# Kernel optimization log

Measured on AMD Instinct MI355X. Metric: run time of the kernel, lower is better.

## Reference

```python
import jax, jax.numpy as jnp
import numpy as np

EMB = 512
HEADS = 8
HEAD_DIM = EMB // HEADS


def setup_inputs() -> dict:
    key = jax.random.key(0)
    ks = jax.random.split(key, 8)
    S, B = 2048, 2
    q = jax.random.normal(ks[0], (S, B, EMB), dtype=jnp.float32)
    k = jax.random.normal(ks[1], (S, B, EMB), dtype=jnp.float32)
    v = jax.random.normal(ks[2], (S, B, EMB), dtype=jnp.float32)
    sc = 1.0 / np.sqrt(HEAD_DIM)
    Wq = jax.random.normal(ks[3], (HEAD_DIM, HEAD_DIM), dtype=jnp.float32) * sc
    Wk = jax.random.normal(ks[4], (HEAD_DIM, HEAD_DIM), dtype=jnp.float32) * sc
    Wv = jax.random.normal(ks[5], (HEAD_DIM, HEAD_DIM), dtype=jnp.float32) * sc
    Wfc = jax.random.normal(ks[6], (EMB, EMB), dtype=jnp.float32) * (1.0 / np.sqrt(EMB))
    bfc = jax.random.normal(ks[7], (EMB,), dtype=jnp.float32) * 0.01
    return {"q": q, "k": k, "v": v, "Wq": Wq, "Wk": Wk, "Wv": Wv, "Wfc": Wfc, "bfc": bfc}


def reference(q, k, v, Wq, Wk, Wv, Wfc, bfc):
    query_len, batch, emb = q.shape
    key_len = k.shape[0]
    value_len = v.shape[0]
    # Faithful to the original: plain reshape (NOT transpose) from [S,B,E] -> [B,H,S,D]
    qh = q.reshape(batch, HEADS, query_len, HEAD_DIM)
    kh = k.reshape(batch, HEADS, key_len, HEAD_DIM)
    vh = v.reshape(batch, HEADS, value_len, HEAD_DIM)
    # torch Linear(head_dim, head_dim, bias=False): y = x @ W.T
    Q = qh @ Wq.T
    K = kh @ Wk.T
    V = vh @ Wv.T
    QK = jnp.einsum('bhqd,bhkd->bhqk', Q, K)  # [B,H,S,S] score matrix (memory-bound)
    filt = jax.nn.softmax(QK / np.sqrt(HEAD_DIM).astype(np.float32), axis=3)
    att = jnp.einsum('bhqk,bhkd->bhqd', filt, V)
    att = att.reshape(query_len, batch, emb)
    return att @ Wfc.T + bfc
```

## Files before the change

### kernel.cpp

```cpp
#include <hip/hip_runtime.h>


typedef __attribute__((ext_vector_type(8))) __bf16 bf16x8;
typedef __attribute__((ext_vector_type(4))) float f32x4;
typedef __attribute__((ext_vector_type(4))) unsigned short u16x4;
typedef __attribute__((ext_vector_type(4))) unsigned int u32x4;
typedef unsigned short u16;
typedef unsigned int u32;

static __device__ __forceinline__ u16 f2bf(float x) {
    u32 u = __float_as_uint(x);
    u += 0x7fff + ((u >> 16) & 1);
    return (u16)(u >> 16);
}
static __device__ __forceinline__ float bf2f(u16 h) {
    return __uint_as_float(((u32)h) << 16);
}
static __device__ __forceinline__ u32 pack2bf(float lo, float hi) {
    u32 a = __float_as_uint(lo), b = __float_as_uint(hi);
    a += 0x7fff + ((a >> 16) & 1);
    b += 0x7fff + ((b >> 16) & 1);
    return (a >> 16) | (b & 0xffff0000u);
}

__global__ __launch_bounds__(256) void proj_kernel(
    const float* __restrict__ q, const float* __restrict__ k, const float* __restrict__ v,
    const float* __restrict__ Wq, const float* __restrict__ Wk, const float* __restrict__ Wv,
    const float* __restrict__ Wfc,
    u16* __restrict__ Qb, u16* __restrict__ Kb, u16* __restrict__ Vt,
    u16* __restrict__ Wb, float* __restrict__ KnSq)
{
    const int mode = blockIdx.z;
    const int t = threadIdx.x;

    if (mode == 3) {
        int i = (blockIdx.x * 256 + t) * 4;
        float4 val = *(const float4*)(Wfc + i);
        u16x4 b = { f2bf(val.x), f2bf(val.y), f2bf(val.z), f2bf(val.w) };
        *(u16x4*)(Wb + i) = b;
        return;
    }

    const float* A = (mode == 0) ? q : (mode == 1) ? k : v;
    const float* W = (mode == 0) ? Wq : (mode == 1) ? Wk : Wv;
    const float osc = (mode == 0) ? 0.18033688011112042f : 1.0f;

    __shared__ alignas(16) u16 Ash[128 * 88];
    __shared__ alignas(16) u16 Wsh[64 * 88];
    __shared__ float red[128];

    const int m0 = blockIdx.x * 128;
    const int w = t >> 6, l = t & 63;
    const int r16 = l & 15, q4 = l >> 4;

    {
        const float4* A4 = (const float4*)(A + (size_t)m0 * 64);
        const int c4 = t & 15;
        #pragma unroll
        for (int i = 0; i < 8; ++i) {
            int row = (t >> 4) + i * 16;
            float4 val = A4[row * 16 + c4];
            u16x4 bb = { f2bf(val.x), f2bf(val.y), f2bf(val.z), f2bf(val.w) };
            *(u16x4*)(Ash + row * 88 + c4 * 4) = bb;
        }
        const float4* W4 = (const float4*)W;
        #pragma unroll
        for (int i = 0; i < 4; ++i) {
            int row = (t >> 4) + i * 16;
            float4 val = W4[row * 16 + c4];
            u16x4 bb = { f2bf(val.x), f2bf(val.y), f2bf(val.z), f2bf(val.w) };
            *(u16x4*)(Wsh + row * 88 + c4 * 4) = bb;
        }
    }
    __syncthreads();

    bf16x8 af[2][2], wf[4][2];
    #pragma unroll
    for (int mc = 0; mc < 2; ++mc)
        #pragma unroll
        for (int kk = 0; kk < 2; ++kk)
            af[mc][kk] = *(const bf16x8*)(Ash + (w * 32 + mc * 16 + r16) * 88 + kk * 32 + q4 * 8);
    #pragma unroll
    for (int nc = 0; nc < 4; ++nc)
        #pragma unroll
        for (int kk = 0; kk < 2; ++kk)
            wf[nc][kk] = *(const bf16x8*)(Wsh + (nc * 16 + r16) * 88 + kk * 32 + q4 * 8);

    f32x4 acc[2][4];
    const f32x4 zero = {0.f, 0.f, 0.f, 0.f};
    #pragma unroll
    for (int mc = 0; mc < 2; ++mc)
        #pragma unroll
        for (int nc = 0; nc < 4; ++nc) {
            acc[mc][nc] = zero;
            acc[mc][nc] = __builtin_amdgcn_mfma_f32_16x16x32_bf16(af[mc][0], wf[nc][0], acc[mc][nc], 0, 0, 0);
            acc[mc][nc] = __builtin_amdgcn_mfma_f32_16x16x32_bf16(af[mc][1], wf[nc][1], acc[mc][nc], 0, 0, 0);
        }

    __syncthreads();

    if (mode < 2) {
        #pragma unroll
        for (int mc = 0; mc < 2; ++mc)
            #pragma unroll
            for (int nc = 0; nc < 4; ++nc)
                #pragma unroll
                for (int r = 0; r < 4; ++r)
                    Ash[(w * 32 + mc * 16 + q4 * 4 + r) * 72 + nc * 16 + r16] = f2bf(acc[mc][nc][r] * osc);
        __syncthreads();
        u16* Out = ((mode == 0) ? Qb : Kb) + (size_t)m0 * 64;
        {
            int row = t >> 1, cbase = (t & 1) * 32;
            #pragma unroll
            for (int i = 0; i < 4; ++i)
                *(u32x4*)(Out + row * 64 + cbase + i * 8) = *(const u32x4*)(Ash + row * 72 + cbase + i * 8);
        }
        if (mode == 1) {
            if (t < 128) {
                float ss = 0.f;
                #pragma unroll
                for (int c = 0; c < 8; ++c) {
                    u32x4 d = *(const u32x4*)(Ash + t * 72 + c * 8);
                    #pragma unroll
                    for (int j = 0; j < 4; ++j) {
                        float lo = bf2f((u16)(d[j] & 0xffff));
                        float hi = bf2f((u16)(d[j] >> 16));
                        ss += lo * lo + hi * hi;
                    }
                }
                red[t] = ss;
            }
            __syncthreads();
            if (t < 64) red[t] = fmaxf(red[t], red[t + 64]);
            __syncthreads();
            if (t < 32) red[t] = fmaxf(red[t], red[t + 32]);
            __syncthreads();
            if (t == 0) {
                float mx = red[0];
                for (int i = 1; i < 32; ++i) mx = fmaxf(mx, red[i]);
                KnSq[blockIdx.x] = mx;
            }
        }
    } else {
        #pragma unroll
        for (int mc = 0; mc < 2; ++mc)
            #pragma unroll
            for (int nc = 0; nc < 4; ++nc)
                #pragma unroll
                for (int r = 0; r < 4; ++r)
                    Ash[(nc * 16 + r16) * 136 + w * 32 + mc * 16 + q4 * 4 + r] = f2bf(acc[mc][nc][r]);
        __syncthreads();
        const int g = m0 >> 11, s0 = m0 & 2047;
        int d = t >> 2, sb = (t & 3) * 32;
        u16* Out = Vt + ((size_t)(g * 64 + d)) * 2048 + s0;
        #pragma unroll
        for (int i = 0; i < 4; ++i)
            *(u32x4*)(Out + sb + i * 8) = *(const u32x4*)(Ash + d * 136 + sb + i * 8);
    }
}

__global__ __launch_bounds__(256) void flash_kernel(
    const u16* __restrict__ Qb, const u16* __restrict__ Kb,
    const u16* __restrict__ Vt, const float* __restrict__ KnSq,
    u16* __restrict__ Att)
{
    const int g = blockIdx.y;
    const int qt = blockIdx.x;
    const int t = threadIdx.x, w = t >> 6, l = t & 63;
    const int r16 = l & 15, q4 = l >> 4;
    const int r7 = r16 & 7;

    __shared__ alignas(16) u16 Kt[2][64 * 64];
    __shared__ alignas(16) u16 Vs[2][64 * 64];
    __shared__ alignas(16) u16 Psh[4][16 * 64];

    const u16* Kg = Kb + ((size_t)g) * 2048 * 64;
    const u16* Vg = Vt + ((size_t)g) * 64 * 2048;

    bf16x8 qb[2];
    {
        const u16* qp = Qb + ((size_t)(g * 2048 + qt * 64 + w * 16 + r16)) * 64 + q4 * 8;
        qb[0] = *(const bf16x8*)qp;
        qb[1] = *(const bf16x8*)(qp + 32);
    }

    float m;
    {
        float kss = KnSq[g * 16 + r16];
        kss = fmaxf(kss, __shfl_xor(kss, 1));
        kss = fmaxf(kss, __shfl_xor(kss, 2));
        kss = fmaxf(kss, __shfl_xor(kss, 4));
        kss = fmaxf(kss, __shfl_xor(kss, 8));
        float ss = 0.f;
        #pragma unroll
        for (int kk = 0; kk < 2; ++kk)
            #pragma unroll
            for (int j = 0; j < 8; ++j) {
                float x = (float)qb[kk][j];
                ss += x * x;
            }
        ss += __shfl_xor(ss, 16);
        ss += __shfl_xor(ss, 32);
        m = sqrtf(ss) * sqrtf(kss) * 1.0002f;
    }

    const int rr = t >> 3, ck = t & 7;
    const int sw0 = (ck ^ (rr & 7)) * 8;

    {
        #pragma unroll
        for (int h = 0; h < 2; ++h) {
            int row = h * 32 + rr;
            *(u32x4*)(&Kt[0][row * 64 + sw0]) = *(const u32x4*)(Kg + (size_t)row * 64 + ck * 8);
            *(u32x4*)(&Vs[0][row * 64 + sw0]) = *(const u32x4*)(Vg + (size_t)row * 2048 + ck * 8);
        }
    }
    __syncthreads();

    f32x4 o[4];
    const f32x4 zero = {0.f, 0.f, 0.f, 0.f};
    #pragma unroll
    for (int dc = 0; dc < 4; ++dc) o[dc] = zero;
    float lsum = 0.f;

    u16* pw = &Psh[w][r16 * 64];
    const int pq_off = (q4 & 1) * 4;
    const int fr0 = ((q4 ^ r7)) * 8;
    const int fr1 = (((q4 + 4) & 7) ^ r7) * 8;

    for (int it = 0; it < 32; ++it) {
        const int cur = it & 1;
        const bool hasn = (it < 31);

        u32x4 knx[2], vnx[2];
        if (hasn) {
            #pragma unroll
            for (int h = 0; h < 2; ++h) {
                int row = h * 32 + rr;
                knx[h] = *(const u32x4*)(Kg + (size_t)((it + 1) * 64 + row) * 64 + ck * 8);
                vnx[h] = *(const u32x4*)(Vg + (size_t)row * 2048 + (it + 1) * 64 + ck * 8);
            }
        }

        const u16* Kc = Kt[cur];
        const u16* Vc = Vs[cur];
        bf16x8 ka[4][2], va[4][2];
        #pragma unroll
        for (int kc = 0; kc < 4; ++kc) {
            ka[kc][0] = *(const bf16x8*)(Kc + (kc * 16 + r16) * 64 + fr0);
            ka[kc][1] = *(const bf16x8*)(Kc + (kc * 16 + r16) * 64 + fr1);
        }
        #pragma unroll
        for (int dc = 0; dc < 4; ++dc) {
            va[dc][0] = *(const bf16x8*)(Vc + (dc * 16 + r16) * 64 + fr0);
            va[dc][1] = *(const bf16x8*)(Vc + (dc * 16 + r16) * 64 + fr1);
        }

        f32x4 s[4];
        #pragma unroll
        for (int kc = 0; kc < 4; ++kc) {
            s[kc] = zero;
            s[kc] = __builtin_amdgcn_mfma_f32_16x16x32_bf16(ka[kc][0], qb[0], s[kc], 0, 0, 0);
            s[kc] = __builtin_amdgcn_mfma_f32_16x16x32_bf16(ka[kc][1], qb[1], s[kc], 0, 0, 0);
        }

        float p[4][4];
        float psum = 0.f;
        #pragma unroll
        for (int kc = 0; kc < 4; ++kc)
            #pragma unroll
            for (int r = 0; r < 4; ++r) {
                p[kc][r] = exp2f(s[kc][r] - m);
                psum += p[kc][r];
            }
        lsum += psum;

        #pragma unroll
        for (int kc = 0; kc < 4; ++kc) {
            uint2 dd = { pack2bf(p[kc][0], p[kc][1]), pack2bf(p[kc][2], p[kc][3]) };
            int sc = ((2 * kc + (q4 >> 1)) ^ r7) * 8 + pq_off;
            *(uint2*)(pw + sc) = dd;
        }
        bf16x8 pb0 = *(const bf16x8*)(pw + fr0);
        bf16x8 pb1 = *(const bf16x8*)(pw + fr1);

        #pragma unroll
        for (int dc = 0; dc < 4; ++dc) {
            o[dc] = __builtin_amdgcn_mfma_f32_16x16x32_bf16(va[dc][0], pb0, o[dc], 0, 0, 0);
            o[dc] = __builtin_amdgcn_mfma_f32_16x16x32_bf16(va[dc][1], pb1, o[dc], 0, 0, 0);
        }

        if (hasn) {
            const int nxt = cur ^ 1;
            #pragma unroll
            for (int h = 0; h < 2; ++h) {
                int row = h * 32 + rr;
                *(u32x4*)(&Kt[nxt][row * 64 + sw0]) = knx[h];
                *(u32x4*)(&Vs[nxt][row * 64 + sw0]) = vnx[h];
            }
        }
        __syncthreads();
    }

    float lt = lsum;
    lt += __shfl_xor(lt, 16);
    lt += __shfl_xor(lt, 32);
    float inv = 1.0f / lt;
    const int qq = qt * 64 + w * 16 + r16;
    u16* orow = Att + ((size_t)(g * 2048 + qq)) * 64;
    #pragma unroll
    for (int dc = 0; dc < 4; ++dc) {
        u16x4 bb = { f2bf(o[dc][0] * inv), f2bf(o[dc][1] * inv),
                     f2bf(o[dc][2] * inv), f2bf(o[dc][3] * inv) };
        *(u16x4*)(orow + dc * 16 + q4 * 4) = bb;
    }
}

__global__ __launch_bounds__(256) void fc_kernel(
    const u16* __restrict__ Att, const u16* __restrict__ Wb,
    const float* __restrict__ bfc, float* __restrict__ out)
{
    __shared__ alignas(16) u16 Ash[2][64 * 64];
    __shared__ alignas(16) u16 Wsh[2][64 * 64];

    const int t = threadIdx.x, w = t >> 6, l = t & 63;
    const int r16 = l & 15, q4 = l >> 4;
    const int r7 = r16 & 7;
    const int m0 = blockIdx.x * 64, n0 = blockIdx.y * 64;

    const int rr = t >> 3, ck = t & 7;
    const int sw0 = (ck ^ (rr & 7)) * 8;
    const int fr0 = (q4 ^ r7) * 8;
    const int fr1 = ((q4 + 4) ^ r7) * 8;

    {
        #pragma unroll
        for (int h = 0; h < 2; ++h) {
            int row = h * 32 + rr;
            *(u32x4*)(&Ash[0][row * 64 + sw0]) = *(const u32x4*)(Att + (size_t)(m0 + row) * 512 + ck * 8);
            *(u32x4*)(&Wsh[0][row * 64 + sw0]) = *(const u32x4*)(Wb + (size_t)(n0 + row) * 512 + ck * 8);
        }
    }
    __syncthreads();

    f32x4 acc[4];
    const f32x4 zero = {0.f, 0.f, 0.f, 0.f};
    #pragma unroll
    for (int nc = 0; nc < 4; ++nc) acc[nc] = zero;

    for (int it = 0; it < 8; ++it) {
        const int cur = it & 1;
        const bool hasn = (it < 7);

        u32x4 anx[2], wnx[2];
        if (hasn) {
            #pragma unroll
            for (int h = 0; h < 2; ++h) {
                int row = h * 32 + rr;
                anx[h] = *(const u32x4*)(Att + (size_t)(m0 + row) * 512 + (it + 1) * 64 + ck * 8);
                wnx[h] = *(const u32x4*)(Wb + (size_t)(n0 + row) * 512 + (it + 1) * 64 + ck * 8);
            }
        }

        bf16x8 af[2], wf[4][2];
        af[0] = *(const bf16x8*)(&Ash[cur][(w * 16 + r16) * 64 + fr0]);
        af[1] = *(const bf16x8*)(&Ash[cur][(w * 16 + r16) * 64 + fr1]);
        #pragma unroll
        for (int nc = 0; nc < 4; ++nc) {
            wf[nc][0] = *(const bf16x8*)(&Wsh[cur][(nc * 16 + r16) * 64 + fr0]);
            wf[nc][1] = *(const bf16x8*)(&Wsh[cur][(nc * 16 + r16) * 64 + fr1]);
        }

        #pragma unroll
        for (int nc = 0; nc < 4; ++nc) {
            acc[nc] = __builtin_amdgcn_mfma_f32_16x16x32_bf16(af[0], wf[nc][0], acc[nc], 0, 0, 0);
            acc[nc] = __builtin_amdgcn_mfma_f32_16x16x32_bf16(af[1], wf[nc][1], acc[nc], 0, 0, 0);
        }

        if (hasn) {
            const int nxt = cur ^ 1;
            #pragma unroll
            for (int h = 0; h < 2; ++h) {
                int row = h * 32 + rr;
                *(u32x4*)(&Ash[nxt][row * 64 + sw0]) = anx[h];
                *(u32x4*)(&Wsh[nxt][row * 64 + sw0]) = wnx[h];
            }
        }
        __syncthreads();
    }

    #pragma unroll
    for (int nc = 0; nc < 4; ++nc) {
        float bb = bfc[n0 + nc * 16 + r16];
        #pragma unroll
        for (int r = 0; r < 4; ++r) {
            int row = m0 + w * 16 + q4 * 4 + r;
            out[(size_t)row * 512 + n0 + nc * 16 + r16] = acc[nc][r] + bb;
        }
    }
}

extern "C" void kernel_launch(void* const* d_in, const int* in_sizes, int n_in,
                              void* d_out, int out_size, void* d_ws, size_t ws_size,
                              hipStream_t stream) {
    (void)in_sizes; (void)n_in; (void)out_size; (void)ws_size;
    const float* q   = (const float*)d_in[0];
    const float* k   = (const float*)d_in[1];
    const float* v   = (const float*)d_in[2];
    const float* Wq  = (const float*)d_in[3];
    const float* Wk  = (const float*)d_in[4];
    const float* Wv  = (const float*)d_in[5];
    const float* Wfc = (const float*)d_in[6];
    const float* bfc = (const float*)d_in[7];
    float* out = (float*)d_out;

    u16* Qb = (u16*)d_ws;
    u16* Kb = Qb + 2097152;
    u16* Vt = Kb + 2097152;
    u16* At = Vt + 2097152;
    u16* Wb = At + 2097152;
    float* KnSq = (float*)((char*)d_ws + 17301504);

    proj_kernel<<<dim3(256, 1, 4), 256, 0, stream>>>(q, k, v, Wq, Wk, Wv, Wfc,
                                                     Qb, Kb, Vt, Wb, KnSq);
    flash_kernel<<<dim3(32, 16), 256, 0, stream>>>(Qb, Kb, Vt, KnSq, At);
    fc_kernel<<<dim3(64, 8), 256, 0, stream>>>(At, Wb, bfc, out);
}
```

Measured before the change: 135.5 us.

## Restructure flash kernel to 32x32 MFMA with key-split warps and smem reduction

The flash attention kernel moves from 16x16x32 MFMA tiles to 32x32x16 MFMA. Each pair of warps now splits a 32-query slice across the two halves of every 64-key tile, and the partial outputs and row sums are combined through shared memory at the end. The output is staged in shared memory so global stores are coalesced, and the grid is flattened so consecutive blocks cover different heads. This aims to cut LDS fragment traffic per FLOP and raise MFMA efficiency, at the cost of an extra cross-warp reduction, more shared memory and more accumulator registers.

```diff
diff --git a/kernel.cpp b/kernel.cpp
--- a/kernel.cpp
+++ b/kernel.cpp
@@ -3,6 +3,7 @@
 
 typedef __attribute__((ext_vector_type(8))) __bf16 bf16x8;
 typedef __attribute__((ext_vector_type(4))) float f32x4;
+typedef __attribute__((ext_vector_type(16))) float f32x16;
 typedef __attribute__((ext_vector_type(4))) unsigned short u16x4;
 typedef __attribute__((ext_vector_type(4))) unsigned int u32x4;
 typedef unsigned short u16;
@@ -164,155 +165,185 @@
     const u16* __restrict__ Vt, const float* __restrict__ KnSq,
     u16* __restrict__ Att)
 {
-    const int g = blockIdx.y;
-    const int qt = blockIdx.x;
+    const int bi = blockIdx.x;
+    const int g = bi & 15;
+    const int qt = bi >> 4;
     const int t = threadIdx.x, w = t >> 6, l = t & 63;
-    const int r16 = l & 15, q4 = l >> 4;
-    const int r7 = r16 & 7;
-
-    __shared__ alignas(16) u16 Kt[2][64 * 64];
-    __shared__ alignas(16) u16 Vs[2][64 * 64];
-    __shared__ alignas(16) u16 Psh[4][16 * 64];
+    const int q5 = l & 31, h = l >> 5;
+    const int qs = w >> 1, kh = w & 1;
+
+    __shared__ alignas(16) unsigned char smem[43008];
+    u16* const base = (u16*)smem;
+    u16* const KT0 = base;
+    u16* const KT1 = base + 4096;
+    u16* const VS0 = base + 8192;
+    u16* const VS1 = base + 12288;
+    u16* const Pw  = base + 16384 + w * 1024;
 
     const u16* Kg = Kb + ((size_t)g) * 2048 * 64;
     const u16* Vg = Vt + ((size_t)g) * 64 * 2048;
 
-    bf16x8 qb[2];
-    {
-        const u16* qp = Qb + ((size_t)(g * 2048 + qt * 64 + w * 16 + r16)) * 64 + q4 * 8;
-        qb[0] = *(const bf16x8*)qp;
-        qb[1] = *(const bf16x8*)(qp + 32);
+    bf16x8 qb[4];
+    {
+        const u16* qp = Qb + ((size_t)(g * 2048 + qt * 64 + qs * 32 + q5)) * 64;
+        #pragma unroll
+        for (int s = 0; s < 4; ++s)
+            qb[s] = *(const bf16x8*)(qp + s * 16 + h * 8);
     }
 
     float m;
     {
-        float kss = KnSq[g * 16 + r16];
+        float kss = KnSq[g * 16 + (l & 15)];
         kss = fmaxf(kss, __shfl_xor(kss, 1));
         kss = fmaxf(kss, __shfl_xor(kss, 2));
         kss = fmaxf(kss, __shfl_xor(kss, 4));
         kss = fmaxf(kss, __shfl_xor(kss, 8));
         float ss = 0.f;
         #pragma unroll
-        for (int kk = 0; kk < 2; ++kk)
+        for (int s = 0; s < 4; ++s)
             #pragma unroll
             for (int j = 0; j < 8; ++j) {
-                float x = (float)qb[kk][j];
+                float x = (float)qb[s][j];
                 ss += x * x;
             }
-        ss += __shfl_xor(ss, 16);
         ss += __shfl_xor(ss, 32);
-        m = sqrtf(ss) * sqrtf(kss) * 1.0002f;
+        m = sqrtf(ss * kss) * 1.0002f;
     }
 
     const int rr = t >> 3, ck = t & 7;
-    const int sw0 = (ck ^ (rr & 7)) * 8;
-
-    {
-        #pragma unroll
-        for (int h = 0; h < 2; ++h) {
-            int row = h * 32 + rr;
-            *(u32x4*)(&Kt[0][row * 64 + sw0]) = *(const u32x4*)(Kg + (size_t)row * 64 + ck * 8);
-            *(u32x4*)(&Vs[0][row * 64 + sw0]) = *(const u32x4*)(Vg + (size_t)row * 2048 + ck * 8);
-        }
-    }
-    __syncthreads();
-
-    f32x4 o[4];
-    const f32x4 zero = {0.f, 0.f, 0.f, 0.f};
-    #pragma unroll
-    for (int dc = 0; dc < 4; ++dc) o[dc] = zero;
-    float lsum = 0.f;
-
-    u16* pw = &Psh[w][r16 * 64];
-    const int pq_off = (q4 & 1) * 4;
-    const int fr0 = ((q4 ^ r7)) * 8;
-    const int fr1 = (((q4 + 4) & 7) ^ r7) * 8;
+    const int swb = (ck ^ (rr & 7)) * 8;
+
+    {
+        #pragma unroll
+        for (int h2 = 0; h2 < 2; ++h2) {
+            int row = h2 * 32 + rr;
+            *(u32x4*)(KT0 + row * 64 + swb) = *(const u32x4*)(Kg + (size_t)row * 64 + ck * 8);
+            *(u32x4*)(VS0 + row * 64 + swb) = *(const u32x4*)(Vg + (size_t)row * 2048 + ck * 8);
+        }
+    }
+    __syncthreads();
+
+    f32x16 o0, o1;
+    #pragma unroll
+    for (int r = 0; r < 16; ++r) { o0[r] = 0.f; o1[r] = 0.f; }
+    float psum = 0.f;
+
+    const int rk = kh * 32 + q5;
+    const int rk7 = rk & 7, q3 = q5 & 3;
 
     for (int it = 0; it < 32; ++it) {
-        const int cur = it & 1;
+        u16* const KTc = (it & 1) ? KT1 : KT0;
+        u16* const VSc = (it & 1) ? VS1 : VS0;
+        u16* const KTn = (it & 1) ? KT0 : KT1;
+        u16* const VSn = (it & 1) ? VS0 : VS1;
         const bool hasn = (it < 31);
 
         u32x4 knx[2], vnx[2];
         if (hasn) {
             #pragma unroll
-            for (int h = 0; h < 2; ++h) {
-                int row = h * 32 + rr;
-                knx[h] = *(const u32x4*)(Kg + (size_t)((it + 1) * 64 + row) * 64 + ck * 8);
-                vnx[h] = *(const u32x4*)(Vg + (size_t)row * 2048 + (it + 1) * 64 + ck * 8);
-            }
-        }
-
-        const u16* Kc = Kt[cur];
-        const u16* Vc = Vs[cur];
-        bf16x8 ka[4][2], va[4][2];
-        #pragma unroll
-        for (int kc = 0; kc < 4; ++kc) {
-            ka[kc][0] = *(const bf16x8*)(Kc + (kc * 16 + r16) * 64 + fr0);
-            ka[kc][1] = *(const bf16x8*)(Kc + (kc * 16 + r16) * 64 + fr1);
-        }
-        #pragma unroll
-        for (int dc = 0; dc < 4; ++dc) {
-            va[dc][0] = *(const bf16x8*)(Vc + (dc * 16 + r16) * 64 + fr0);
-            va[dc][1] = *(const bf16x8*)(Vc + (dc * 16 + r16) * 64 + fr1);
-        }
-
-        f32x4 s[4];
-        #pragma unroll
-        for (int kc = 0; kc < 4; ++kc) {
-            s[kc] = zero;
-            s[kc] = __builtin_amdgcn_mfma_f32_16x16x32_bf16(ka[kc][0], qb[0], s[kc], 0, 0, 0);
-            s[kc] = __builtin_amdgcn_mfma_f32_16x16x32_bf16(ka[kc][1], qb[1], s[kc], 0, 0, 0);
-        }
-
-        float p[4][4];
-        float psum = 0.f;
-        #pragma unroll
-        for (int kc = 0; kc < 4; ++kc)
-            #pragma unroll
-            for (int r = 0; r < 4; ++r) {
-                p[kc][r] = exp2f(s[kc][r] - m);
-                psum += p[kc][r];
-            }
-        lsum += psum;
-
-        #pragma unroll
-        for (int kc = 0; kc < 4; ++kc) {
-            uint2 dd = { pack2bf(p[kc][0], p[kc][1]), pack2bf(p[kc][2], p[kc][3]) };
-            int sc = ((2 * kc + (q4 >> 1)) ^ r7) * 8 + pq_off;
-            *(uint2*)(pw + sc) = dd;
-        }
-        bf16x8 pb0 = *(const bf16x8*)(pw + fr0);
-        bf16x8 pb1 = *(const bf16x8*)(pw + fr1);
-
-        #pragma unroll
-        for (int dc = 0; dc < 4; ++dc) {
-            o[dc] = __builtin_amdgcn_mfma_f32_16x16x32_bf16(va[dc][0], pb0, o[dc], 0, 0, 0);
-            o[dc] = __builtin_amdgcn_mfma_f32_16x16x32_bf16(va[dc][1], pb1, o[dc], 0, 0, 0);
+            for (int h2 = 0; h2 < 2; ++h2) {
+                int row = h2 * 32 + rr;
+                knx[h2] = *(const u32x4*)(Kg + (size_t)((it + 1) * 64 + row) * 64 + ck * 8);
+                vnx[h2] = *(const u32x4*)(Vg + (size_t)row * 2048 + (it + 1) * 64 + ck * 8);
+            }
+        }
+
+        bf16x8 ka0 = *(const bf16x8*)(KTc + rk * 64 + (((0 + h) ^ rk7) * 8));
+        bf16x8 ka1 = *(const bf16x8*)(KTc + rk * 64 + (((2 + h) ^ rk7) * 8));
+        bf16x8 ka2 = *(const bf16x8*)(KTc + rk * 64 + (((4 + h) ^ rk7) * 8));
+        bf16x8 ka3 = *(const bf16x8*)(KTc + rk * 64 + (((6 + h) ^ rk7) * 8));
+        f32x16 sa, sb;
+        #pragma unroll
+        for (int r = 0; r < 16; ++r) { sa[r] = 0.f; sb[r] = 0.f; }
+        sa = __builtin_amdgcn_mfma_f32_32x32x16_bf16(ka0, qb[0], sa, 0, 0, 0);
+        sb = __builtin_amdgcn_mfma_f32_32x32x16_bf16(ka2, qb[2], sb, 0, 0, 0);
+        sa = __builtin_amdgcn_mfma_f32_32x32x16_bf16(ka1, qb[1], sa, 0, 0, 0);
+        sb = __builtin_amdgcn_mfma_f32_32x32x16_bf16(ka3, qb[3], sb, 0, 0, 0);
+
+        float p[16];
+        float ps = 0.f;
+        #pragma unroll
+        for (int r = 0; r < 16; ++r) {
+            p[r] = exp2f((sa[r] + sb[r]) - m);
+            ps += p[r];
+        }
+        psum += ps;
+
+        #pragma unroll
+        for (int u = 0; u < 4; ++u) {
+            uint2 dd = { pack2bf(p[4 * u + 0], p[4 * u + 1]),
+                         pack2bf(p[4 * u + 2], p[4 * u + 3]) };
+            *(uint2*)(Pw + q5 * 32 + ((u ^ q3) * 8) + 4 * h) = dd;
+        }
+        bf16x8 pb0 = *(const bf16x8*)(Pw + q5 * 32 + (((0 + h) ^ q3) * 8));
+        bf16x8 pb1 = *(const bf16x8*)(Pw + q5 * 32 + (((2 + h) ^ q3) * 8));
+
+        {
+            int rv = q5;
+            int rv7 = rv & 7;
+            bf16x8 va0 = *(const bf16x8*)(VSc + rv * 64 + (((4 * kh + 0 + h) ^ rv7) * 8));
+            bf16x8 va1 = *(const bf16x8*)(VSc + rv * 64 + (((4 * kh + 2 + h) ^ rv7) * 8));
+            o0 = __builtin_amdgcn_mfma_f32_32x32x16_bf16(va0, pb0, o0, 0, 0, 0);
+            o0 = __builtin_amdgcn_mfma_f32_32x32x16_bf16(va1, pb1, o0, 0, 0, 0);
+        }
+        {
+            int rv = 32 + q5;
+            int rv7 = rv & 7;
+            bf16x8 va0 = *(const bf16x8*)(VSc + rv * 64 + (((4 * kh + 0 + h) ^ rv7) * 8));
+            bf16x8 va1 = *(const bf16x8*)(VSc + rv * 64 + (((4 * kh + 2 + h) ^ rv7) * 8));
+            o1 = __builtin_amdgcn_mfma_f32_32x32x16_bf16(va0, pb0, o1, 0, 0, 0);
+            o1 = __builtin_amdgcn_mfma_f32_32x32x16_bf16(va1, pb1, o1, 0, 0, 0);
         }
 
         if (hasn) {
-            const int nxt = cur ^ 1;
-            #pragma unroll
-            for (int h = 0; h < 2; ++h) {
-                int row = h * 32 + rr;
-                *(u32x4*)(&Kt[nxt][row * 64 + sw0]) = knx[h];
-                *(u32x4*)(&Vs[nxt][row * 64 + sw0]) = vnx[h];
+            #pragma unroll
+            for (int h2 = 0; h2 < 2; ++h2) {
+                int row = h2 * 32 + rr;
+                *(u32x4*)(KTn + row * 64 + swb) = knx[h2];
+                *(u32x4*)(VSn + row * 64 + swb) = vnx[h2];
             }
         }
         __syncthreads();
     }
 
-    float lt = lsum;
-    lt += __shfl_xor(lt, 16);
-    lt += __shfl_xor(lt, 32);
-    float inv = 1.0f / lt;
-    const int qq = qt * 64 + w * 16 + r16;
-    u16* orow = Att + ((size_t)(g * 2048 + qq)) * 64;
-    #pragma unroll
-    for (int dc = 0; dc < 4; ++dc) {
-        u16x4 bb = { f2bf(o[dc][0] * inv), f2bf(o[dc][1] * inv),
-                     f2bf(o[dc][2] * inv), f2bf(o[dc][3] * inv) };
-        *(u16x4*)(orow + dc * 16 + q4 * 4) = bb;
+    float psq = psum + __shfl_xor(psum, 32);
+
+    float* const Fsh = (float*)smem;
+    float* const LsF = (float*)(smem + 16896);
+    u16*  const Osh = base + 12288;
+
+    if (kh == 1) {
+        float* fp = Fsh + (qs * 64 + l) * 33;
+        #pragma unroll
+        for (int r = 0; r < 16; ++r) { fp[r] = o0[r]; fp[16 + r] = o1[r]; }
+        fp[32] = psq;
+        LsF[qs * 64 + l] = psq;
+    }
+    __syncthreads();
+    if (kh == 0) {
+        const float* fp = Fsh + (qs * 64 + l) * 33;
+        float inv = 1.0f / (psq + LsF[qs * 64 + l]);
+        const int qloc = qs * 32 + q5;
+        #pragma unroll
+        for (int u = 0; u < 4; ++u) {
+            u16x4 b0 = { f2bf((o0[4*u+0] + fp[4*u+0]) * inv),
+                         f2bf((o0[4*u+1] + fp[4*u+1]) * inv),
+                         f2bf((o0[4*u+2] + fp[4*u+2]) * inv),
+                         f2bf((o0[4*u+3] + fp[4*u+3]) * inv) };
+            *(u16x4*)(Osh + qloc * 72 + 8 * u + 4 * h) = b0;
+            u16x4 b1 = { f2bf((o1[4*u+0] + fp[16+4*u+0]) * inv),
+                         f2bf((o1[4*u+1] + fp[16+4*u+1]) * inv),
+                         f2bf((o1[4*u+2] + fp[16+4*u+2]) * inv),
+                         f2bf((o1[4*u+3] + fp[16+4*u+3]) * inv) };
+            *(u16x4*)(Osh + qloc * 72 + 32 + 8 * u + 4 * h) = b1;
+        }
+    }
+    __syncthreads();
+    {
+        int row = t >> 2, cb = (t & 3) * 16;
+        u16* dst = Att + ((size_t)(g * 2048 + qt * 64 + row)) * 64 + cb;
+        *(u32x4*)(dst)     = *(const u32x4*)(Osh + row * 72 + cb);
+        *(u32x4*)(dst + 8) = *(const u32x4*)(Osh + row * 72 + cb + 8);
     }
 }
 
@@ -423,6 +454,6 @@
 
     proj_kernel<<<dim3(256, 1, 4), 256, 0, stream>>>(q, k, v, Wq, Wk, Wv, Wfc,
                                                      Qb, Kb, Vt, Wb, KnSq);
-    flash_kernel<<<dim3(32, 16), 256, 0, stream>>>(Qb, Kb, Vt, KnSq, At);
+    flash_kernel<<<dim3(512), 256, 0, stream>>>(Qb, Kb, Vt, KnSq, At);
     fc_kernel<<<dim3(64, 8), 256, 0, stream>>>(At, Wb, bfc, out);
 }
```

Result: slower. 140.0 us (+3.3%).
